# Performance work log

Measured on AMD Instinct MI355X. Metric: run time of the kernel, lower is better.

## Reference

```python
import jax, jax.numpy as jnp
import numpy as np


def _pairwise_mse_gram(x):
    """G[i, j] = mean_d (x[i, d] - x[j, d])**2, computed in closed form.

    Replaces the original O(N^2) Python double loop over F.mse_loss with a
    single GEMM: |x_i|^2 + |x_j|^2 - 2 x_i . x_j, divided by D.
    """
    x = x.reshape(x.shape[0], -1)            # [N, D]
    D = x.shape[1]
    sq = jnp.sum(x * x, axis=1)              # [N]
    gram = x @ x.T                           # [N, N] GEMM
    return (sq[:, None] + sq[None, :] - 2.0 * gram) / D


def setup_inputs() -> dict:
    key = jax.random.key(0)
    k1, k2 = jax.random.split(key)
    fm_s = jax.random.normal(k1, (1024, 64, 16, 16), dtype=jnp.float32)
    fm_t = jax.random.normal(k2, (1024, 64, 16, 16), dtype=jnp.float32)
    return {"fm_s": fm_s, "fm_t": fm_t}


def reference(fm_s, fm_t):
    # Faithful to the original source, including its bug: the second double
    # loop writes the teacher pairwise-MSE matrix into G_s (overwriting the
    # student one entirely), while G_t stays all-zeros. Hence the final loss
    # is mse(pairwise_mse_gram(fm_t), 0) and fm_s does not affect the output.
    G_s = _pairwise_mse_gram(fm_t)           # [N, N]
    G_t = jnp.zeros_like(G_s)
    return jnp.mean((G_s - G_t) ** 2)
```

## Files before the change

### kernel.cpp

```cpp
#include <hip/hip_runtime.h>
#include <hip/hip_bf16.h>
#include <stdint.h>

#define N_ROWS 1024
#define KDIM   16384
#define SPLITK 16
#define KBLK   (KDIM / SPLITK)
#define BK     32
#define NITER  (KBLK / BK)

typedef __attribute__((ext_vector_type(8))) __bf16 bf16x8;
typedef __attribute__((ext_vector_type(4))) float  f32x4;

#define GLOBAL_AS __attribute__((address_space(1)))
#define LDS_AS    __attribute__((address_space(3)))

#define WAITCNT_VM(N) __builtin_amdgcn_s_waitcnt(0x0F70 | (N))

__device__ __forceinline__ void block_barrier() {
    asm volatile("" ::: "memory");
    __builtin_amdgcn_s_barrier();
    asm volatile("" ::: "memory");
}

__device__ __constant__ unsigned char T_I[36] = {
    0,0,0,0,0,0,0,0, 1,1,1,1,1,1,1, 2,2,2,2,2,2, 3,3,3,3,3, 4,4,4,4, 5,5,5, 6,6, 7};
__device__ __constant__ unsigned char T_J[36] = {
    0,1,2,3,4,5,6,7, 1,2,3,4,5,6,7, 2,3,4,5,6,7, 3,4,5,6,7, 4,5,6,7, 5,6,7, 6,7, 7};

__device__ __forceinline__ unsigned short f32_to_bf16_rne(float f) {
    unsigned int u = __float_as_uint(f);
    unsigned int lsb = (u >> 16) & 1u;
    u += 0x7fffu + lsb;
    return (unsigned short)(u >> 16);
}

__global__ __launch_bounds__(256) void cast_sq_kernel(
        const float* __restrict__ X, unsigned short* __restrict__ Xb,
        float* __restrict__ sq) {
    const int row = blockIdx.x;
    const float4* src = (const float4*)(X + (size_t)row * KDIM);
    uint2* dst = (uint2*)(Xb + (size_t)row * KDIM);
    float ss = 0.f;
#pragma unroll
    for (int c = 0; c < 16; ++c) {
        int idx = c * 256 + threadIdx.x;
        float4 v = src[idx];
        ss += v.x * v.x + v.y * v.y + v.z * v.z + v.w * v.w;
        uint2 p;
        p.x = (unsigned int)f32_to_bf16_rne(v.x) | ((unsigned int)f32_to_bf16_rne(v.y) << 16);
        p.y = (unsigned int)f32_to_bf16_rne(v.z) | ((unsigned int)f32_to_bf16_rne(v.w) << 16);
        dst[idx] = p;
    }
#pragma unroll
    for (int o = 32; o; o >>= 1) ss += __shfl_down(ss, o, 64);
    __shared__ float red[4];
    int lane = threadIdx.x & 63, wv = threadIdx.x >> 6;
    if (lane == 0) red[wv] = ss;
    __syncthreads();
    if (threadIdx.x == 0) sq[row] = red[0] + red[1] + red[2] + red[3];
}

__global__ __launch_bounds__(256) void gram_gemm_kernel(
        const unsigned short* __restrict__ Xb, unsigned short* __restrict__ P) {
    __shared__ unsigned short SH[3 * 8192];

    const int ti = T_I[blockIdx.x];
    const int tj = T_J[blockIdx.x];
    const int row0 = ti * 128;
    const int col0 = tj * 128;
    const int kbeg = blockIdx.y * KBLK;

    const int tid  = threadIdx.x;
    const int lane = tid & 63;
    const int wv   = tid >> 6;
    const int wm   = (wv >> 1) * 64;
    const int wn   = (wv & 1) * 64;
    const int lr   = lane & 15;
    const int lq   = lane >> 4;
    const int soff = (lq ^ ((lr >> 1) & 3)) * 8;

    const int c0 = tid, c1 = 256 + tid;
    const int r0 = c0 >> 2, j0 = c0 & 3, js0 = j0 ^ ((r0 >> 1) & 3);
    const int r1 = c1 >> 2, j1 = c1 & 3, js1 = j1 ^ ((r1 >> 1) & 3);
    const unsigned short* gA0 = Xb + (size_t)(row0 + r0) * KDIM + kbeg + js0 * 8;
    const unsigned short* gA1 = Xb + (size_t)(row0 + r1) * KDIM + kbeg + js1 * 8;
    const unsigned short* gB0 = Xb + (size_t)(col0 + r0) * KDIM + kbeg + js0 * 8;
    const unsigned short* gB1 = Xb + (size_t)(col0 + r1) * KDIM + kbeg + js1 * 8;

    f32x4 acc[4][4] = {};

#define STAGE(ph, kk)                                                          \
    do {                                                                       \
        unsigned short* b = &SH[(ph) * 8192];                                  \
        __builtin_amdgcn_global_load_lds((GLOBAL_AS void*)(void*)(gA0 + (kk)), \
                                         (LDS_AS void*)&b[c0 * 8], 16, 0, 0);  \
        __builtin_amdgcn_global_load_lds((GLOBAL_AS void*)(void*)(gA1 + (kk)), \
                                         (LDS_AS void*)&b[c1 * 8], 16, 0, 0);  \
        __builtin_amdgcn_global_load_lds((GLOBAL_AS void*)(void*)(gB0 + (kk)), \
                                         (LDS_AS void*)&b[4096 + c0 * 8], 16, 0, 0); \
        __builtin_amdgcn_global_load_lds((GLOBAL_AS void*)(void*)(gB1 + (kk)), \
                                         (LDS_AS void*)&b[4096 + c1 * 8], 16, 0, 0); \
    } while (0)

#define COMPUTE(ph)                                                            \
    do {                                                                       \
        const unsigned short* b = &SH[(ph) * 8192];                            \
        bf16x8 af[4], bq[4];                                                   \
        _Pragma("unroll")                                                      \
        for (int i = 0; i < 4; ++i)                                            \
            af[i] = *(const bf16x8*)&b[(wm + i * 16 + lr) * 32 + soff];        \
        _Pragma("unroll")                                                      \
        for (int j = 0; j < 4; ++j)                                            \
            bq[j] = *(const bf16x8*)&b[4096 + (wn + j * 16 + lr) * 32 + soff]; \
        _Pragma("unroll")                                                      \
        for (int i = 0; i < 4; ++i)                                            \
            _Pragma("unroll")                                                  \
            for (int j = 0; j < 4; ++j)                                        \
                acc[i][j] = __builtin_amdgcn_mfma_f32_16x16x32_bf16(           \
                    af[i], bq[j], acc[i][j], 0, 0, 0);                         \
    } while (0)

    STAGE(0, 0);
    STAGE(1, BK);
    STAGE(2, 2 * BK);

    int ph = 0;
    for (int k = 0; k < NITER - 2; ++k) {
        WAITCNT_VM(8);
        block_barrier();
        COMPUTE(ph);
        block_barrier();
        if (k + 3 < NITER) STAGE(ph, (k + 3) * BK);
        ph = (ph == 2) ? 0 : ph + 1;
    }
    WAITCNT_VM(4);
    block_barrier();
    COMPUTE(ph);
    block_barrier();
    ph = (ph == 2) ? 0 : ph + 1;
    WAITCNT_VM(0);
    block_barrier();
    COMPUTE(ph);
#undef STAGE
#undef COMPUTE

    unsigned short* dst = P + ((size_t)blockIdx.x * SPLITK + blockIdx.y) * 16384;
    const int rbase = wm + lq * 4;
    const int cbase = wn + lr;
#pragma unroll
    for (int i = 0; i < 4; ++i)
#pragma unroll
        for (int j = 0; j < 4; ++j)
#pragma unroll
            for (int r = 0; r < 4; ++r) {
                int e = (rbase + i * 16 + r) * 128 + (cbase + j * 16);
                dst[e] = f32_to_bf16_rne(acc[i][j][r]);
            }
}

__global__ __launch_bounds__(256) void loss_kernel(
        const unsigned short* __restrict__ P, const float* __restrict__ sq,
        float* __restrict__ out) {
    const float invD = 1.0f / (float)KDIM;
    const int TOT = 36 * 128 * 128;
    float acc = 0.f;
    for (int u = blockIdx.x * 256 + threadIdx.x; u < TOT; u += gridDim.x * 256) {
        int t = u >> 14;
        int e = u & 16383;
        int i = T_I[t] * 128 + (e >> 7);
        int j = T_J[t] * 128 + (e & 127);
        const unsigned short* pb = P + (size_t)t * SPLITK * 16384 + e;
        float g = 0.f;
#pragma unroll
        for (int s = 0; s < SPLITK; ++s)
            g += __uint_as_float((unsigned int)pb[s * 16384] << 16);
        float v = (sq[i] + sq[j] - 2.0f * g) * invD;
        float w = (T_I[t] == T_J[t]) ? 1.0f : 2.0f;
        acc += w * v * v;
    }
#pragma unroll
    for (int o = 32; o; o >>= 1) acc += __shfl_down(acc, o, 64);
    __shared__ float red[4];
    int lane = threadIdx.x & 63, wv = threadIdx.x >> 6;
    if (lane == 0) red[wv] = acc;
    __syncthreads();
    if (threadIdx.x == 0) {
        float total = red[0] + red[1] + red[2] + red[3];
        atomicAdd(out, total * (1.0f / ((float)N_ROWS * (float)N_ROWS)));
    }
}

extern "C" void kernel_launch(void* const* d_in, const int* in_sizes, int n_in,
                              void* d_out, int out_size, void* d_ws, size_t ws_size,
                              hipStream_t stream) {
    const float* fm_t = (const float*)d_in[1];
    float* out = (float*)d_out;

    char* ws = (char*)d_ws;
    unsigned short* Xb = (unsigned short*)ws;
    unsigned short* P  = (unsigned short*)(ws + (size_t)N_ROWS * KDIM * 2);
    float* sq = (float*)(ws + (size_t)N_ROWS * KDIM * 2
                            + (size_t)36 * SPLITK * 16384 * 2);

    hipMemsetAsync(out, 0, sizeof(float), stream);

    cast_sq_kernel<<<dim3(N_ROWS), 256, 0, stream>>>(fm_t, Xb, sq);
    gram_gemm_kernel<<<dim3(36, SPLITK), 256, 0, stream>>>(Xb, P);
    loss_kernel<<<dim3(512), 256, 0, stream>>>(P, sq, out);
}
```

Baseline: 189.6 us.

## Split cast kernel per half-row, single-barrier GEMM pipeline, vectorize loss reduction

The cast kernel now uses two blocks per row and accumulates the squared norms with atomics, so sq must be zeroed first. The GEMM main loop changes from two barriers per step with a prefetch depth of three to one barrier per step, issuing the next-but-one stage before compute. The loss kernel reads 8 bf16 partials per thread as a vector instead of a grid-stride scalar loop, and is launched with exactly enough blocks to cover the work. Together these target barrier overhead and memory access efficiency, at the cost of an extra memset and atomic contention.

```diff
diff --git a/kernel.cpp b/kernel.cpp
--- a/kernel.cpp
+++ b/kernel.cpp
@@ -10,6 +10,7 @@
 #define NITER  (KBLK / BK)
 
 typedef __attribute__((ext_vector_type(8))) __bf16 bf16x8;
+typedef __attribute__((ext_vector_type(8))) unsigned short ushort8;
 typedef __attribute__((ext_vector_type(4))) float  f32x4;
 
 #define GLOBAL_AS __attribute__((address_space(1)))
@@ -38,12 +39,13 @@
 __global__ __launch_bounds__(256) void cast_sq_kernel(
         const float* __restrict__ X, unsigned short* __restrict__ Xb,
         float* __restrict__ sq) {
-    const int row = blockIdx.x;
-    const float4* src = (const float4*)(X + (size_t)row * KDIM);
-    uint2* dst = (uint2*)(Xb + (size_t)row * KDIM);
+    const int row = blockIdx.x >> 1;
+    const int seg = blockIdx.x & 1;
+    const float4* src = (const float4*)(X + (size_t)row * KDIM) + seg * 2048;
+    uint2* dst = (uint2*)(Xb + (size_t)row * KDIM) + seg * 2048;
     float ss = 0.f;
 #pragma unroll
-    for (int c = 0; c < 16; ++c) {
+    for (int c = 0; c < 8; ++c) {
         int idx = c * 256 + threadIdx.x;
         float4 v = src[idx];
         ss += v.x * v.x + v.y * v.y + v.z * v.z + v.w * v.w;
@@ -58,7 +60,7 @@
     int lane = threadIdx.x & 63, wv = threadIdx.x >> 6;
     if (lane == 0) red[wv] = ss;
     __syncthreads();
-    if (threadIdx.x == 0) sq[row] = red[0] + red[1] + red[2] + red[3];
+    if (threadIdx.x == 0) atomicAdd(&sq[row], red[0] + red[1] + red[2] + red[3]);
 }
 
 __global__ __launch_bounds__(256) void gram_gemm_kernel(
@@ -123,25 +125,17 @@
 
     STAGE(0, 0);
     STAGE(1, BK);
-    STAGE(2, 2 * BK);
-
-    int ph = 0;
-    for (int k = 0; k < NITER - 2; ++k) {
-        WAITCNT_VM(8);
+
+    int cph = 0, wph = 2;
+    for (int k = 0; k < NITER; ++k) {
+        if (k < NITER - 1) WAITCNT_VM(4);
+        else               WAITCNT_VM(0);
         block_barrier();
-        COMPUTE(ph);
-        block_barrier();
-        if (k + 3 < NITER) STAGE(ph, (k + 3) * BK);
-        ph = (ph == 2) ? 0 : ph + 1;
-    }
-    WAITCNT_VM(4);
-    block_barrier();
-    COMPUTE(ph);
-    block_barrier();
-    ph = (ph == 2) ? 0 : ph + 1;
-    WAITCNT_VM(0);
-    block_barrier();
-    COMPUTE(ph);
+        if (k + 2 < NITER) STAGE(wph, (k + 2) * BK);
+        COMPUTE(cph);
+        cph = (cph == 2) ? 0 : cph + 1;
+        wph = (wph == 2) ? 0 : wph + 1;
+    }
 #undef STAGE
 #undef COMPUTE
 
@@ -163,20 +157,27 @@
         const unsigned short* __restrict__ P, const float* __restrict__ sq,
         float* __restrict__ out) {
     const float invD = 1.0f / (float)KDIM;
-    const int TOT = 36 * 128 * 128;
+    const int u  = blockIdx.x * 256 + threadIdx.x;
+    const int t  = u >> 11;
+    const int e0 = (u & 2047) * 8;
+
+    const unsigned short* pb = P + (size_t)t * SPLITK * 16384 + e0;
+    float g[8] = {};
+#pragma unroll
+    for (int s = 0; s < SPLITK; ++s) {
+        ushort8 v = *(const ushort8*)(pb + s * 16384);
+#pragma unroll
+        for (int x = 0; x < 8; ++x)
+            g[x] += __uint_as_float(((unsigned int)v[x]) << 16);
+    }
+    const int i  = T_I[t] * 128 + (e0 >> 7);
+    const int jb = T_J[t] * 128 + (e0 & 127);
+    const float w = (T_I[t] == T_J[t]) ? 1.0f : 2.0f;
+    const float sqi = sq[i];
     float acc = 0.f;
-    for (int u = blockIdx.x * 256 + threadIdx.x; u < TOT; u += gridDim.x * 256) {
-        int t = u >> 14;
-        int e = u & 16383;
-        int i = T_I[t] * 128 + (e >> 7);
-        int j = T_J[t] * 128 + (e & 127);
-        const unsigned short* pb = P + (size_t)t * SPLITK * 16384 + e;
-        float g = 0.f;
-#pragma unroll
-        for (int s = 0; s < SPLITK; ++s)
-            g += __uint_as_float((unsigned int)pb[s * 16384] << 16);
-        float v = (sq[i] + sq[j] - 2.0f * g) * invD;
-        float w = (T_I[t] == T_J[t]) ? 1.0f : 2.0f;
+#pragma unroll
+    for (int x = 0; x < 8; ++x) {
+        float v = (sqi + sq[jb + x] - 2.0f * g[x]) * invD;
         acc += w * v * v;
     }
 #pragma unroll
@@ -204,8 +205,9 @@
                             + (size_t)36 * SPLITK * 16384 * 2);
 
     hipMemsetAsync(out, 0, sizeof(float), stream);
-
-    cast_sq_kernel<<<dim3(N_ROWS), 256, 0, stream>>>(fm_t, Xb, sq);
+    hipMemsetAsync(sq, 0, N_ROWS * sizeof(float), stream);
+
+    cast_sq_kernel<<<dim3(2 * N_ROWS), 256, 0, stream>>>(fm_t, Xb, sq);
     gram_gemm_kernel<<<dim3(36, SPLITK), 256, 0, stream>>>(Xb, P);
-    loss_kernel<<<dim3(512), 256, 0, stream>>>(P, sq, out);
-}
+    loss_kernel<<<dim3(288), 256, 0, stream>>>(P, sq, out);
+}
```

New measurement: 184.6 us. 1.03x faster.
